# Optimization experiments

Hardware: AMD Instinct MI355X
Metric: run time of the kernel (lower is better)

The kernel has to match this reference:

```python
import jax, jax.numpy as jnp
import numpy as np

KV_H, Q_H, ATT_H = 256, 256, 128
B, S, SQ = 2, 1024, 512

def setup_inputs() -> dict:
    key = jax.random.key(0)
    ks = jax.random.split(key, 8)
    sc = lambda d: 1.0 / np.sqrt(d)
    return {
        "attention_kv": jax.random.normal(ks[0], (B, S, KV_H), dtype=jnp.float32),
        "attention_query": jax.random.normal(ks[1], (B, SQ, Q_H), dtype=jnp.float32),
        "W_kv": jax.random.uniform(ks[2], (KV_H, ATT_H), jnp.float32, -sc(KV_H), sc(KV_H)),
        "b_kv": jax.random.uniform(ks[3], (ATT_H,), jnp.float32, -sc(KV_H), sc(KV_H)),
        "W_q": jax.random.uniform(ks[4], (Q_H, ATT_H), jnp.float32, -sc(Q_H), sc(Q_H)),
        "b_q": jax.random.uniform(ks[5], (ATT_H,), jnp.float32, -sc(Q_H), sc(Q_H)),
        "w_v": jax.random.uniform(ks[6], (ATT_H,), jnp.float32, -sc(ATT_H), sc(ATT_H)),
        "b_v": jax.random.uniform(ks[7], (), jnp.float32, -sc(ATT_H), sc(ATT_H)),
    }

def reference(attention_kv, attention_query, W_kv, b_kv, W_q, b_q, w_v, b_v):
    # proj_kv: (B, S, A); proj_q: (B, Sq, A)
    proj_kv = jnp.einsum('bsh,ha->bsa', attention_kv, W_kv) + b_kv
    proj_q = jnp.einsum('bqh,ha->bqa', attention_query, W_q) + b_q
    # broadcast add + tanh -> (B, Sq, S, A)
    hidden = jnp.tanh(proj_kv[:, None, :, :] + proj_q[:, :, None, :])
    # scalar score per (b, q, s)
    attention_score = jnp.einsum('bqsa,a->bqs', hidden, w_v) + b_v
    attention_weight = jax.nn.softmax(attention_score, axis=-1)
    # weighted sum over kv sequence -> (B, Sq, KV_H)
    attention_output = jnp.einsum('bqs,bsh->bqh', attention_weight, attention_kv)
    return attention_output, attention_weight
```

## Files before the change

kernel.cpp:

```cpp
#include <hip/hip_runtime.h>

#define NB   2
#define SKV  1024
#define NSQ  512
#define HIN  256
#define HA   128

#define KSC   2.8853900817779268f
#define LOG2E 1.4426950408889634f

__global__ __launch_bounds__(128) void proj_kernel(
    const float* __restrict__ kv,
    const float* __restrict__ qy,
    const float* __restrict__ Wkv,
    const float* __restrict__ bkv,
    const float* __restrict__ Wq,
    const float* __restrict__ bq,
    float* __restrict__ ek,
    float* __restrict__ eq)
{
    const int t  = threadIdx.x;
    const int r0 = blockIdx.x * 8;
    const bool is_q = (r0 >= NB * SKV);
    const float* __restrict__ src = is_q ? (qy + (size_t)(r0 - NB * SKV) * HIN)
                                         : (kv + (size_t)r0 * HIN);
    const float* __restrict__ W  = is_q ? Wq : Wkv;
    const float* __restrict__ bs = is_q ? bq : bkv;
    float* __restrict__ dst = is_q ? (eq + (size_t)(r0 - NB * SKV) * HA)
                                   : (ek + (size_t)r0 * HA);

    float a[8];
    #pragma unroll
    for (int i = 0; i < 8; ++i) a[i] = 0.f;

    const float4* __restrict__ s4 = (const float4*)src;
    #pragma unroll 2
    for (int h4 = 0; h4 < 64; ++h4) {
        float4 r[8];
        #pragma unroll
        for (int i = 0; i < 8; ++i) r[i] = s4[(size_t)i * 64 + h4];
        #pragma unroll
        for (int j = 0; j < 4; ++j) {
            const float w = W[(size_t)(h4 * 4 + j) * HA + t];
            #pragma unroll
            for (int i = 0; i < 8; ++i)
                a[i] = fmaf(((const float*)&r[i])[j], w, a[i]);
        }
    }
    const float bb = bs[t];
    #pragma unroll
    for (int i = 0; i < 8; ++i)
        dst[(size_t)i * HA + t] = __builtin_amdgcn_exp2f((a[i] + bb) * KSC);
}

__global__ __launch_bounds__(1024) void attn_kernel(
    const float* __restrict__ ek,
    const float* __restrict__ eq,
    const float* __restrict__ wv,
    const float* __restrict__ bv,
    const float* __restrict__ kv,
    float* __restrict__ out)
{
    __shared__ __align__(16) float wt_s[SKV][4];
    __shared__ __align__(16) float part[16][4][HIN];
    __shared__ float red[2][4][16];

    const int tid  = threadIdx.x;
    const int lane = tid & 63, wid = tid >> 6;
    const int bq0  = blockIdx.x * 4;
    const int b    = bq0 >> 9;

    const float4* __restrict__ eq4 = (const float4*)(eq + (size_t)bq0 * HA);
    const float4* __restrict__ wv4 = (const float4*)wv;

    float W0 = bv[0];
    #pragma unroll 8
    for (int i = 0; i < 32; ++i) {
        const float4 w = wv4[i];
        W0 += (w.x + w.y) + (w.z + w.w);
    }

    const int s = tid;
    const float4* __restrict__ ek4 =
        (const float4*)(ek + ((size_t)(b * SKV + s)) * HA);
    float acc0 = 0.f, acc1 = 0.f, acc2 = 0.f, acc3 = 0.f;

    #pragma unroll 4
    for (int a4 = 0; a4 < 32; ++a4) {
        const float4 E = ek4[a4];
        const float4 w = wv4[a4];

#define PAIR_Q(ACC, QIDX)                                                     \
        {                                                                     \
            const float4 Q = eq4[(QIDX) * 32 + a4];      \
            float u  = fmaf(E.x, Q.x, 1.f);                                   \
            float v  = fmaf(E.y, Q.y, 1.f);                                   \
            float n  = fmaf(w.x, v, w.y * u);                                 \
            ACC = fmaf(n, __builtin_amdgcn_rcpf(u * v), ACC);                 \
            float u2 = fmaf(E.z, Q.z, 1.f);                                   \
            float v2 = fmaf(E.w, Q.w, 1.f);                                   \
            float n2 = fmaf(w.z, v2, w.w * u2);                               \
            ACC = fmaf(n2, __builtin_amdgcn_rcpf(u2 * v2), ACC);              \
        }
        PAIR_Q(acc0, 0)
        PAIR_Q(acc1, 1)
        PAIR_Q(acc2, 2)
        PAIR_Q(acc3, 3)
#undef PAIR_Q
    }

    float sc[4];
    sc[0] = fmaf(-2.f, acc0, W0);
    sc[1] = fmaf(-2.f, acc1, W0);
    sc[2] = fmaf(-2.f, acc2, W0);
    sc[3] = fmaf(-2.f, acc3, W0);

    #pragma unroll
    for (int q = 0; q < 4; ++q) {
        float m = sc[q];
        #pragma unroll
        for (int o = 32; o > 0; o >>= 1) m = fmaxf(m, __shfl_down(m, o));
        if (lane == 0) red[0][q][wid] = m;
    }
    __syncthreads();
    float M[4];
    #pragma unroll
    for (int q = 0; q < 4; ++q) {
        float m = red[0][q][0];
        #pragma unroll
        for (int i = 1; i < 16; ++i) m = fmaxf(m, red[0][q][i]);
        M[q] = m;
    }
    float e[4];
    #pragma unroll
    for (int q = 0; q < 4; ++q) {
        e[q] = __builtin_amdgcn_exp2f((sc[q] - M[q]) * LOG2E);
        float sum = e[q];
        #pragma unroll
        for (int o = 32; o > 0; o >>= 1) sum += __shfl_down(sum, o);
        if (lane == 0) red[1][q][wid] = sum;
    }
    __syncthreads();
    float wgt[4];
    #pragma unroll
    for (int q = 0; q < 4; ++q) {
        float d = red[1][q][0];
        #pragma unroll
        for (int i = 1; i < 16; ++i) d += red[1][q][i];
        wgt[q] = e[q] * __builtin_amdgcn_rcpf(d);
    }

    float* __restrict__ outw = out + (size_t)NB * NSQ * HIN;
    *(float4*)&wt_s[s][0] = make_float4(wgt[0], wgt[1], wgt[2], wgt[3]);
    #pragma unroll
    for (int q = 0; q < 4; ++q)
        outw[(size_t)(bq0 + q) * SKV + s] = wgt[q];
    __syncthreads();

    {
        const int g = wid;
        float4 ac0 = {0,0,0,0}, ac1 = {0,0,0,0}, ac2 = {0,0,0,0}, ac3 = {0,0,0,0};
        const float4* __restrict__ kvb =
            (const float4*)(kv + (size_t)(b * SKV + g * 64) * HIN);
        #pragma unroll 4
        for (int i = 0; i < 64; ++i) {
            const float4 w4 = *((const float4*)&wt_s[g * 64 + i][0]);
            const float4 v  = kvb[(size_t)i * 64 + lane];
            ac0.x = fmaf(w4.x, v.x, ac0.x); ac0.y = fmaf(w4.x, v.y, ac0.y);
            ac0.z = fmaf(w4.x, v.z, ac0.z); ac0.w = fmaf(w4.x, v.w, ac0.w);
            ac1.x = fmaf(w4.y, v.x, ac1.x); ac1.y = fmaf(w4.y, v.y, ac1.y);
            ac1.z = fmaf(w4.y, v.z, ac1.z); ac1.w = fmaf(w4.y, v.w, ac1.w);
            ac2.x = fmaf(w4.z, v.x, ac2.x); ac2.y = fmaf(w4.z, v.y, ac2.y);
            ac2.z = fmaf(w4.z, v.z, ac2.z); ac2.w = fmaf(w4.z, v.w, ac2.w);
            ac3.x = fmaf(w4.w, v.x, ac3.x); ac3.y = fmaf(w4.w, v.y, ac3.y);
            ac3.z = fmaf(w4.w, v.z, ac3.z); ac3.w = fmaf(w4.w, v.w, ac3.w);
        }
        ((float4*)part[g][0])[lane] = ac0;
        ((float4*)part[g][1])[lane] = ac1;
        ((float4*)part[g][2])[lane] = ac2;
        ((float4*)part[g][3])[lane] = ac3;
    }
    __syncthreads();
    {
        const int q = tid >> 8, h = tid & 255;
        float v = 0.f;
        #pragma unroll
        for (int g2 = 0; g2 < 16; ++g2) v += part[g2][q][h];
        out[(size_t)(bq0 + q) * HIN + h] = v;
    }
}

extern "C" void kernel_launch(void* const* d_in, const int* in_sizes, int n_in,
                              void* d_out, int out_size, void* d_ws, size_t ws_size,
                              hipStream_t stream) {
    (void)in_sizes; (void)n_in; (void)out_size; (void)ws_size;
    const float* kv  = (const float*)d_in[0];
    const float* qy  = (const float*)d_in[1];
    const float* Wkv = (const float*)d_in[2];
    const float* bkv = (const float*)d_in[3];
    const float* Wq  = (const float*)d_in[4];
    const float* bq  = (const float*)d_in[5];
    const float* wv  = (const float*)d_in[6];
    const float* bv  = (const float*)d_in[7];

    float* ek = (float*)d_ws;
    float* eqp = ek + (size_t)NB * SKV * HA;
    float* out = (float*)d_out;

    hipLaunchKernelGGL(proj_kernel, dim3((NB * SKV + NB * NSQ) / 8), dim3(128), 0, stream,
                       kv, qy, Wkv, bkv, Wq, bq, ek, eqp);
    hipLaunchKernelGGL(attn_kernel, dim3(NB * NSQ / 4), dim3(1024), 0, stream,
                       ek, eqp, wv, bv, kv, out);
}
```

Measured before the change: 118.5 us.

## Transpose key projections, split weighted-sum into separate kernel, stage operands in LDS

The key projection is stored in an a4-major, s-minor layout so that each thread's float4 loads in the score loop coalesce across the sequence dimension. Query and w_v vectors are staged in shared memory. The softmax drops the constant bias terms and uses a min reduction on the raw accumulator. The weighted sum over kv moves to a new kernel that processes 8 queries per block and half of the hidden dim, which raises kv reuse. The proj kernel now uses 512 threads with rows staged in LDS. The cost is an extra launch and a round-trip of the weights through global memory.

```diff
diff --git a/kernel.cpp b/kernel.cpp
--- a/kernel.cpp
+++ b/kernel.cpp
@@ -7,62 +7,68 @@
 #define HA   128
 
 #define KSC   2.8853900817779268f
-#define LOG2E 1.4426950408889634f
-
-__global__ __launch_bounds__(128) void proj_kernel(
+
+__global__ __launch_bounds__(512) void proj_kernel(
     const float* __restrict__ kv,
     const float* __restrict__ qy,
     const float* __restrict__ Wkv,
     const float* __restrict__ bkv,
     const float* __restrict__ Wq,
     const float* __restrict__ bq,
-    float* __restrict__ ek,
+    float* __restrict__ ekT,
     float* __restrict__ eq)
 {
+    __shared__ __align__(16) float rowf[8][HIN];
     const int t  = threadIdx.x;
+    const int a  = t & 127;
+    const int rh = t >> 7;
     const int r0 = blockIdx.x * 8;
     const bool is_q = (r0 >= NB * SKV);
     const float* __restrict__ src = is_q ? (qy + (size_t)(r0 - NB * SKV) * HIN)
                                          : (kv + (size_t)r0 * HIN);
     const float* __restrict__ W  = is_q ? Wq : Wkv;
     const float* __restrict__ bs = is_q ? bq : bkv;
-    float* __restrict__ dst = is_q ? (eq + (size_t)(r0 - NB * SKV) * HA)
-                                   : (ek + (size_t)r0 * HA);
-
-    float a[8];
-    #pragma unroll
-    for (int i = 0; i < 8; ++i) a[i] = 0.f;
-
-    const float4* __restrict__ s4 = (const float4*)src;
-    #pragma unroll 2
+
+    ((float4*)rowf)[t] = ((const float4*)src)[t];
+    __syncthreads();
+
+    float a0 = 0.f, a1 = 0.f;
+    const int ra = rh * 2, rb = rh * 2 + 1;
+    #pragma unroll 4
     for (int h4 = 0; h4 < 64; ++h4) {
-        float4 r[8];
-        #pragma unroll
-        for (int i = 0; i < 8; ++i) r[i] = s4[(size_t)i * 64 + h4];
+        const float4 r4a = ((const float4*)rowf[ra])[h4];
+        const float4 r4b = ((const float4*)rowf[rb])[h4];
         #pragma unroll
         for (int j = 0; j < 4; ++j) {
-            const float w = W[(size_t)(h4 * 4 + j) * HA + t];
-            #pragma unroll
-            for (int i = 0; i < 8; ++i)
-                a[i] = fmaf(((const float*)&r[i])[j], w, a[i]);
+            const float w = W[(size_t)(h4 * 4 + j) * HA + a];
+            a0 = fmaf(((const float*)&r4a)[j], w, a0);
+            a1 = fmaf(((const float*)&r4b)[j], w, a1);
         }
     }
-    const float bb = bs[t];
-    #pragma unroll
-    for (int i = 0; i < 8; ++i)
-        dst[(size_t)i * HA + t] = __builtin_amdgcn_exp2f((a[i] + bb) * KSC);
+    const float bb = bs[a];
+    const float e0 = __builtin_amdgcn_exp2f((a0 + bb) * KSC);
+    const float e1 = __builtin_amdgcn_exp2f((a1 + bb) * KSC);
+    if (is_q) {
+        const int r = r0 - NB * SKV;
+        eq[(size_t)(r + ra) * HA + a] = e0;
+        eq[(size_t)(r + rb) * HA + a] = e1;
+    } else {
+        const int bI = r0 >> 10, s0 = r0 & 1023;
+        float* __restrict__ p =
+            ekT + ((size_t)(bI * 32 + (a >> 2)) * SKV + s0) * 4 + (a & 3);
+        p[(size_t)ra * 4] = e0;
+        p[(size_t)rb * 4] = e1;
+    }
 }
 
 __global__ __launch_bounds__(1024) void attn_kernel(
-    const float* __restrict__ ek,
+    const float* __restrict__ ekT,
     const float* __restrict__ eq,
     const float* __restrict__ wv,
-    const float* __restrict__ bv,
-    const float* __restrict__ kv,
     float* __restrict__ out)
 {
-    __shared__ __align__(16) float wt_s[SKV][4];
-    __shared__ __align__(16) float part[16][4][HIN];
+    __shared__ __align__(16) float eq_s[4][HA];
+    __shared__ __align__(16) float wv_s[HA];
     __shared__ float red[2][4][16];
 
     const int tid  = threadIdx.x;
@@ -70,56 +76,41 @@
     const int bq0  = blockIdx.x * 4;
     const int b    = bq0 >> 9;
 
-    const float4* __restrict__ eq4 = (const float4*)(eq + (size_t)bq0 * HA);
-    const float4* __restrict__ wv4 = (const float4*)wv;
-
-    float W0 = bv[0];
-    #pragma unroll 8
-    for (int i = 0; i < 32; ++i) {
-        const float4 w = wv4[i];
-        W0 += (w.x + w.y) + (w.z + w.w);
-    }
-
-    const int s = tid;
-    const float4* __restrict__ ek4 =
-        (const float4*)(ek + ((size_t)(b * SKV + s)) * HA);
-    float acc0 = 0.f, acc1 = 0.f, acc2 = 0.f, acc3 = 0.f;
+    if (tid < 512) ((float*)eq_s)[tid] = eq[(size_t)bq0 * HA + tid];
+    else if (tid < 640) wv_s[tid - 512] = wv[tid - 512];
+    __syncthreads();
+
+    const float4* __restrict__ E4 =
+        (const float4*)ekT + (size_t)b * 32 * SKV + tid;
+    float t0 = 0.f, t1 = 0.f, t2 = 0.f, t3 = 0.f;
 
     #pragma unroll 4
     for (int a4 = 0; a4 < 32; ++a4) {
-        const float4 E = ek4[a4];
-        const float4 w = wv4[a4];
-
-#define PAIR_Q(ACC, QIDX)                                                     \
+        const float4 E = E4[(size_t)a4 * SKV];
+        const float4 w = ((const float4*)wv_s)[a4];
+
+#define PQ(ACC, QI)                                                           \
         {                                                                     \
-            const float4 Q = eq4[(QIDX) * 32 + a4];      \
+            const float4 Q = ((const float4*)eq_s[QI])[a4];    \
             float u  = fmaf(E.x, Q.x, 1.f);                                   \
             float v  = fmaf(E.y, Q.y, 1.f);                                   \
-            float n  = fmaf(w.x, v, w.y * u);                                 \
-            ACC = fmaf(n, __builtin_amdgcn_rcpf(u * v), ACC);                 \
+            ACC = fmaf(fmaf(w.x, v, w.y * u),                                 \
+                       __builtin_amdgcn_rcpf(u * v), ACC);                    \
             float u2 = fmaf(E.z, Q.z, 1.f);                                   \
             float v2 = fmaf(E.w, Q.w, 1.f);                                   \
-            float n2 = fmaf(w.z, v2, w.w * u2);                               \
-            ACC = fmaf(n2, __builtin_amdgcn_rcpf(u2 * v2), ACC);              \
+            ACC = fmaf(fmaf(w.z, v2, w.w * u2),                               \
+                       __builtin_amdgcn_rcpf(u2 * v2), ACC);                  \
         }
-        PAIR_Q(acc0, 0)
-        PAIR_Q(acc1, 1)
-        PAIR_Q(acc2, 2)
-        PAIR_Q(acc3, 3)
-#undef PAIR_Q
-    }
-
-    float sc[4];
-    sc[0] = fmaf(-2.f, acc0, W0);
-    sc[1] = fmaf(-2.f, acc1, W0);
-    sc[2] = fmaf(-2.f, acc2, W0);
-    sc[3] = fmaf(-2.f, acc3, W0);
-
-    #pragma unroll
-    for (int q = 0; q < 4; ++q) {
-        float m = sc[q];
-        #pragma unroll
-        for (int o = 32; o > 0; o >>= 1) m = fmaxf(m, __shfl_down(m, o));
+        PQ(t0, 0) PQ(t1, 1) PQ(t2, 2) PQ(t3, 3)
+#undef PQ
+    }
+
+    float tq[4] = {t0, t1, t2, t3};
+    #pragma unroll
+    for (int q = 0; q < 4; ++q) {
+        float m = tq[q];
+        #pragma unroll
+        for (int o = 32; o > 0; o >>= 1) m = fminf(m, __shfl_down(m, o));
         if (lane == 0) red[0][q][wid] = m;
     }
     __syncthreads();
@@ -128,65 +119,83 @@
     for (int q = 0; q < 4; ++q) {
         float m = red[0][q][0];
         #pragma unroll
-        for (int i = 1; i < 16; ++i) m = fmaxf(m, red[0][q][i]);
+        for (int i = 1; i < 16; ++i) m = fminf(m, red[0][q][i]);
         M[q] = m;
     }
     float e[4];
     #pragma unroll
     for (int q = 0; q < 4; ++q) {
-        e[q] = __builtin_amdgcn_exp2f((sc[q] - M[q]) * LOG2E);
+        e[q] = __builtin_amdgcn_exp2f((M[q] - tq[q]) * KSC);
         float sum = e[q];
         #pragma unroll
         for (int o = 32; o > 0; o >>= 1) sum += __shfl_down(sum, o);
         if (lane == 0) red[1][q][wid] = sum;
     }
     __syncthreads();
-    float wgt[4];
+    float* __restrict__ outw = out + (size_t)NB * NSQ * HIN;
     #pragma unroll
     for (int q = 0; q < 4; ++q) {
         float d = red[1][q][0];
         #pragma unroll
         for (int i = 1; i < 16; ++i) d += red[1][q][i];
-        wgt[q] = e[q] * __builtin_amdgcn_rcpf(d);
-    }
-
-    float* __restrict__ outw = out + (size_t)NB * NSQ * HIN;
-    *(float4*)&wt_s[s][0] = make_float4(wgt[0], wgt[1], wgt[2], wgt[3]);
-    #pragma unroll
-    for (int q = 0; q < 4; ++q)
-        outw[(size_t)(bq0 + q) * SKV + s] = wgt[q];
-    __syncthreads();
-
-    {
-        const int g = wid;
-        float4 ac0 = {0,0,0,0}, ac1 = {0,0,0,0}, ac2 = {0,0,0,0}, ac3 = {0,0,0,0};
-        const float4* __restrict__ kvb =
-            (const float4*)(kv + (size_t)(b * SKV + g * 64) * HIN);
-        #pragma unroll 4
-        for (int i = 0; i < 64; ++i) {
-            const float4 w4 = *((const float4*)&wt_s[g * 64 + i][0]);
-            const float4 v  = kvb[(size_t)i * 64 + lane];
-            ac0.x = fmaf(w4.x, v.x, ac0.x); ac0.y = fmaf(w4.x, v.y, ac0.y);
-            ac0.z = fmaf(w4.x, v.z, ac0.z); ac0.w = fmaf(w4.x, v.w, ac0.w);
-            ac1.x = fmaf(w4.y, v.x, ac1.x); ac1.y = fmaf(w4.y, v.y, ac1.y);
-            ac1.z = fmaf(w4.y, v.z, ac1.z); ac1.w = fmaf(w4.y, v.w, ac1.w);
-            ac2.x = fmaf(w4.z, v.x, ac2.x); ac2.y = fmaf(w4.z, v.y, ac2.y);
-            ac2.z = fmaf(w4.z, v.z, ac2.z); ac2.w = fmaf(w4.z, v.w, ac2.w);
-            ac3.x = fmaf(w4.w, v.x, ac3.x); ac3.y = fmaf(w4.w, v.y, ac3.y);
-            ac3.z = fmaf(w4.w, v.z, ac3.z); ac3.w = fmaf(w4.w, v.w, ac3.w);
+        outw[(size_t)(bq0 + q) * SKV + tid] = e[q] * __builtin_amdgcn_rcpf(d);
+    }
+}
+
+__global__ __launch_bounds__(512) void out_kernel(
+    const float* __restrict__ kv,
+    const float* __restrict__ outw,
+    float* __restrict__ out)
+{
+    __shared__ __align__(16) float wtT[SKV][8];
+    __shared__ __align__(16) float part[16][8][HA];
+
+    const int t  = threadIdx.x;
+    const int qg = blockIdx.x >> 1, hh = blockIdx.x & 1;
+    const int b  = qg >> 6;
+
+    #pragma unroll
+    for (int j = 0; j < 16; ++j) {
+        const int idx = j * 512 + t, q = idx >> 10, s = idx & 1023;
+        wtT[s][q] = outw[(size_t)(qg * 8 + q) * SKV + s];
+    }
+    __syncthreads();
+
+    const int h4 = t & 31, sg = t >> 5;
+    const float4* __restrict__ kv4 =
+        (const float4*)kv + ((size_t)(b * SKV + sg * 64)) * 64 + hh * 32 + h4;
+
+    float4 ac[8];
+    #pragma unroll
+    for (int q = 0; q < 8; ++q) ac[q] = make_float4(0.f, 0.f, 0.f, 0.f);
+
+    #pragma unroll 2
+    for (int i = 0; i < 64; ++i) {
+        const int s = sg * 64 + i;
+        const float4 v  = kv4[(size_t)i * 64];
+        const float4 wA = ((const float4*)wtT[s])[0];
+        const float4 wB = ((const float4*)wtT[s])[1];
+        #pragma unroll
+        for (int q = 0; q < 4; ++q) {
+            const float wa = ((const float*)&wA)[q];
+            ac[q].x = fmaf(wa, v.x, ac[q].x); ac[q].y = fmaf(wa, v.y, ac[q].y);
+            ac[q].z = fmaf(wa, v.z, ac[q].z); ac[q].w = fmaf(wa, v.w, ac[q].w);
+            const float wb = ((const float*)&wB)[q];
+            ac[q+4].x = fmaf(wb, v.x, ac[q+4].x); ac[q+4].y = fmaf(wb, v.y, ac[q+4].y);
+            ac[q+4].z = fmaf(wb, v.z, ac[q+4].z); ac[q+4].w = fmaf(wb, v.w, ac[q+4].w);
         }
-        ((float4*)part[g][0])[lane] = ac0;
-        ((float4*)part[g][1])[lane] = ac1;
-        ((float4*)part[g][2])[lane] = ac2;
-        ((float4*)part[g][3])[lane] = ac3;
-    }
-    __syncthreads();
-    {
-        const int q = tid >> 8, h = tid & 255;
+    }
+    #pragma unroll
+    for (int q = 0; q < 8; ++q) ((float4*)part[sg][q])[h4] = ac[q];
+    __syncthreads();
+
+    #pragma unroll
+    for (int k = 0; k < 2; ++k) {
+        const int idx = k * 512 + t, q = idx >> 7, h = idx & 127;
         float v = 0.f;
         #pragma unroll
-        for (int g2 = 0; g2 < 16; ++g2) v += part[g2][q][h];
-        out[(size_t)(bq0 + q) * HIN + h] = v;
+        for (int g = 0; g < 16; ++g) v += part[g][q][h];
+        out[(size_t)(qg * 8 + q) * HIN + hh * HA + h] = v;
     }
 }
 
@@ -201,14 +210,15 @@
     const float* Wq  = (const float*)d_in[4];
     const float* bq  = (const float*)d_in[5];
     const float* wv  = (const float*)d_in[6];
-    const float* bv  = (const float*)d_in[7];
-
-    float* ek = (float*)d_ws;
-    float* eqp = ek + (size_t)NB * SKV * HA;
+    float* ekT = (float*)d_ws;
+    float* eqp = ekT + (size_t)NB * SKV * HA;
     float* out = (float*)d_out;
-
-    hipLaunchKernelGGL(proj_kernel, dim3((NB * SKV + NB * NSQ) / 8), dim3(128), 0, stream,
-                       kv, qy, Wkv, bkv, Wq, bq, ek, eqp);
+    float* outw = out + (size_t)NB * NSQ * HIN;
+
+    hipLaunchKernelGGL(proj_kernel, dim3((NB * SKV + NB * NSQ) / 8), dim3(512), 0, stream,
+                       kv, qy, Wkv, bkv, Wq, bq, ekT, eqp);
     hipLaunchKernelGGL(attn_kernel, dim3(NB * NSQ / 4), dim3(1024), 0, stream,
-                       ek, eqp, wv, bv, kv, out);
-}
+                       ekT, eqp, wv, out);
+    hipLaunchKernelGGL(out_kernel, dim3(NB * NSQ / 4), dim3(512), 0, stream,
+                       kv, outw, out);
+}
```

New measurement: 114.2 us. 1.04x faster.
